# Kernel optimization log

Hardware: AMD Instinct MI355X
Metric: run time of the kernel (lower is better)

## Reference

```python
import jax, jax.numpy as jnp
import numpy as np

# config constants
B, S, H = 4, 2048, 1024
E = 8                 # n_routed_experts
M = 512               # moe_intermediate_size
K = 2                 # num_experts_per_tok
N_SHARED = 2
SM = M * N_SHARED     # shared expert intermediate
G = 64                # gene_size
GE_TEMP = 1.0
ALPHA = 0.001         # aux_loss_alpha
SEQ_AUX = True
NORM_TOPK = True
COS_TEMP = 0.78
CONS_ALPHA = 0.01
LEAKY_SLOPE = 0.01
EPS_COS = 1e-8


def setup_inputs() -> dict:
    key = jax.random.key(0)
    ks = jax.random.split(key, 12)
    sh = 1.0 / np.sqrt(H)
    sm = 1.0 / np.sqrt(M)
    ssm = 1.0 / np.sqrt(SM)
    sg = 1.0 / np.sqrt(G)
    return {
        "hidden_states": jax.random.normal(ks[0], (B, S, H), jnp.float32),
        "g": jax.random.normal(ks[1], (B, G), jnp.float32),
        "wt": jax.random.uniform(ks[2], (E, H), jnp.float32, -sh, sh),   # gate weight_token
        "wg": jax.random.uniform(ks[3], (E, G), jnp.float32, -sg, sg),   # gate weight_gene
        "w_gate": jax.random.uniform(ks[4], (E, H, M), jnp.float32, -sh, sh),
        "w_up": jax.random.uniform(ks[5], (E, H, M), jnp.float32, -sh, sh),
        "w_down": jax.random.uniform(ks[6], (E, M, H), jnp.float32, -sm, sm),
        "sw_gate": jax.random.uniform(ks[7], (H, SM), jnp.float32, -sh, sh),
        "sw_up": jax.random.uniform(ks[8], (H, SM), jnp.float32, -sh, sh),
        "sw_down": jax.random.uniform(ks[9], (SM, H), jnp.float32, -ssm, ssm),
    }


def _leaky(x):
    return jnp.where(x >= 0, x, LEAKY_SLOPE * x)


def _moe_forward(hidden_states, g, wt, wg, w_gate, w_up, w_down, sw_gate, sw_up, sw_down):
    b, s, h = hidden_states.shape
    x = hidden_states.reshape(-1, h)                    # [T, H], T = b*s
    T = x.shape[0]

    # ---- gate ----
    logits_h = x @ wt.T                                 # [T, E]
    logits_g = g @ wg.T                                 # [b, E]
    logits_g = jnp.repeat(logits_g, s, axis=0)          # [T, E]
    logits = (logits_h + logits_g / GE_TEMP) / (1.0 + 1.0 / GE_TEMP)
    scores = jax.nn.softmax(logits, axis=-1)            # [T, E]
    topk_w, topk_idx = jax.lax.top_k(scores, K)         # [T, K]
    if K > 1 and NORM_TOPK:
        topk_w = topk_w / (topk_w.sum(-1, keepdims=True) + 1e-20)

    # aux loss (seq_aux=True)
    onehot = jax.nn.one_hot(topk_idx.reshape(b, s * K), E, dtype=jnp.float32)  # [b, s*K, E]
    ce = onehot.sum(1) / (s * K / E)                    # [b, E]
    aux_loss = (ce * scores.reshape(b, s, E).mean(1)).sum(1).mean() * ALPHA

    # ---- routed experts: dense stacked compute, then gather ----
    gp = _leaky(jnp.einsum('th,ehm->etm', x, w_gate))   # [E, T, M]
    up = jnp.einsum('th,ehm->etm', x, w_up)
    y_all = jnp.einsum('etm,emh->eth', gp * up, w_down) # [E, T, H]
    y_sel = y_all[topk_idx, jnp.arange(T)[:, None], :]  # [T, K, H]
    y = (y_sel * topk_w[..., None]).sum(1).reshape(b, s, h)

    # ---- shared expert ----
    p = (_leaky(hidden_states @ sw_gate) * (hidden_states @ sw_up)) @ sw_down
    y = y + p

    # consistency cosine loss
    num = jnp.sum(y * p, -1)
    den = jnp.maximum(jnp.linalg.norm(y, axis=-1), EPS_COS) * jnp.maximum(jnp.linalg.norm(p, axis=-1), EPS_COS)
    closs = CONS_ALPHA * jnp.mean((num / den) / (1.0 + COS_TEMP))
    return y, aux_loss + closs


def reference(hidden_states, g, wt, wg, w_gate, w_up, w_down, sw_gate, sw_up, sw_down):
    y, _ = _moe_forward(hidden_states, g, wt, wg, w_gate, w_up, w_down, sw_gate, sw_up, sw_down)
    return y
```

## Files before the change

### kernel.cpp

```cpp
#include <hip/hip_runtime.h>
#include <stdint.h>

#define T_TOK 8192
#define H_DIM 1024
#define M_DIM 512
#define SM_DIM 1024
#define E_NUM 8
#define S_SEQ 2048
#define G_DIM 64
#define NASSIGN 16384
#define NSLOT (NASSIGN + E_NUM * 256)
#define MAX_TILES (NASSIGN / 256 + E_NUM)
#define NBLK_PLACE (NASSIGN / 256)

typedef float f32x4 __attribute__((ext_vector_type(4)));
typedef short bf16x8 __attribute__((ext_vector_type(8)));

struct TileDesc { int base; int expert; int nrows; };

#define WAITCNT_VM6 asm volatile("s_waitcnt vmcnt(6)" ::: "memory")
#define WAITCNT_VM4 asm volatile("s_waitcnt vmcnt(4)" ::: "memory")
#define WAITCNT_VM2 asm volatile("s_waitcnt vmcnt(2)" ::: "memory")
#define WAITCNT_VM0 asm volatile("s_waitcnt vmcnt(0)" ::: "memory")

static __device__ __forceinline__ ushort f2b(float f) {
  union { float f; uint32_t u; } a; a.f = f;
  uint32_t r = a.u + 0x7fffu + ((a.u >> 16) & 1u);
  return (ushort)(r >> 16);
}
static __device__ __forceinline__ float b2f(ushort u) {
  union { uint32_t u; float f; } a; a.u = ((uint32_t)u) << 16;
  return a.f;
}
static __device__ __forceinline__ int imin(int a, int b) { return a < b ? a : b; }

static __device__ __forceinline__ void gll16(const void* g, void* l) {
  __builtin_amdgcn_global_load_lds(
      (const __attribute__((address_space(1))) void*)g,
      (__attribute__((address_space(3))) void*)l, 16, 0, 0);
}
static __device__ __forceinline__ int xcd_remap(int wg, int nwg) {
  return (wg & 7) * (nwg >> 3) + (wg >> 3);
}

__global__ __launch_bounds__(256) void prep_kernel(
    const float* __restrict__ x, const float* __restrict__ wt, const float* __restrict__ g,
    const float* __restrict__ wgm,
    const float* __restrict__ w_gate, const float* __restrict__ w_up,
    const float* __restrict__ w_down, const float* __restrict__ sw_gate,
    const float* __restrict__ sw_up, const float* __restrict__ sw_down,
    ushort* __restrict__ wg_t, ushort* __restrict__ wu_t,
    ushort* __restrict__ wd_t, ushort* __restrict__ swg_t,
    ushort* __restrict__ swu_t, ushort* __restrict__ swd_t,
    ushort* __restrict__ xb, int* __restrict__ tidx, float* __restrict__ tw,
    int* __restrict__ bcount) {
  __shared__ float tile[32][33];
  int id = blockIdx.x;
  if (id < 15360) {
    int tx = threadIdx.x & 31, ty = threadIdx.x >> 5;
    const float* src; ushort* dst; int R, C, t;
    if (id < 4096)        { src = w_gate;  dst = wg_t;  R = 1024; C = 512;  t = id; }
    else if (id < 8192)   { src = w_up;    dst = wu_t;  R = 1024; C = 512;  t = id - 4096; }
    else if (id < 12288)  { src = w_down;  dst = wd_t;  R = 512;  C = 1024; t = id - 8192; }
    else if (id < 13312)  { src = sw_gate; dst = swg_t; R = 1024; C = 1024; t = id - 12288; }
    else if (id < 14336)  { src = sw_up;   dst = swu_t; R = 1024; C = 1024; t = id - 13312; }
    else                  { src = sw_down; dst = swd_t; R = 1024; C = 1024; t = id - 14336; }
    int tc = C >> 5;
    int tpm = (R >> 5) * tc;
    int e = t / tpm, tt = t % tpm;
    int c0 = (tt % tc) * 32, r0 = (tt / tc) * 32;
    size_t bo = (size_t)e * R * C;
    src += bo; dst += bo;
#pragma unroll
    for (int i = 0; i < 4; ++i)
      tile[ty + i * 8][tx] = src[(size_t)(r0 + ty + i * 8) * C + c0 + tx];
    __syncthreads();
#pragma unroll
    for (int i = 0; i < 4; ++i)
      dst[(size_t)(c0 + ty + i * 8) * R + r0 + tx] = f2b(tile[tx][ty + i * 8]);
    return;
  }
  int id2 = id - 15360;
  int wv = threadIdx.x >> 6, lane = threadIdx.x & 63;
  int t = id2 * 4 + wv;
  const float4* xr4 = (const float4*)x + (size_t)t * 256;
  ushort4* xb4 = (ushort4*)xb + (size_t)t * 256;
  float a[E_NUM];
#pragma unroll
  for (int e = 0; e < E_NUM; ++e) a[e] = 0.f;
#pragma unroll
  for (int j = 0; j < 4; ++j) {
    float4 v = xr4[lane + 64 * j];
    ushort4 o;
    o.x = f2b(v.x); o.y = f2b(v.y); o.z = f2b(v.z); o.w = f2b(v.w);
    xb4[lane + 64 * j] = o;
#pragma unroll
    for (int e = 0; e < E_NUM; ++e) {
      float4 wv4 = ((const float4*)(wt + (size_t)e * H_DIM))[lane + 64 * j];
      a[e] += v.x * wv4.x + v.y * wv4.y + v.z * wv4.z + v.w * wv4.w;
    }
  }
#pragma unroll
  for (int e = 0; e < E_NUM; ++e)
    for (int off = 32; off; off >>= 1) a[e] += __shfl_xor(a[e], off, 64);
  float lge = 0.f;
  int b = t / S_SEQ;
  if (lane < E_NUM) {
    const float* gv = g + b * G_DIM;
    const float* wv2 = wgm + lane * G_DIM;
    for (int i = 0; i < G_DIM; ++i) lge += gv[i] * wv2[i];
  }
  float l[E_NUM];
#pragma unroll
  for (int e = 0; e < E_NUM; ++e) l[e] = 0.5f * (a[e] + __shfl(lge, e, 64));
  if (lane == 0) {
    int i1 = 0; float b1 = l[0];
#pragma unroll
    for (int e = 1; e < E_NUM; ++e) if (l[e] > b1) { b1 = l[e]; i1 = e; }
    int i2 = -1; float b2 = -1e30f;
#pragma unroll
    for (int e = 0; e < E_NUM; ++e) if (e != i1 && l[e] > b2) { b2 = l[e]; i2 = e; }
    float e2 = expf(b2 - b1);
    float inv = 1.f / (1.f + e2);
    tidx[t * 2] = i1; tidx[t * 2 + 1] = i2;
    tw[t * 2] = inv;  tw[t * 2 + 1] = e2 * inv;
    int chunk = t >> 7;
    atomicAdd(&bcount[chunk * E_NUM + i1], 1);
    atomicAdd(&bcount[chunk * E_NUM + i2], 1);
  }
}

__global__ __launch_bounds__(256) void place2_kernel(
    const int* __restrict__ tidx, const int* __restrict__ bcount,
    int* __restrict__ perm, int* __restrict__ slot_of,
    TileDesc* __restrict__ desc, int* __restrict__ ndesc) {
  __shared__ int cnt[E_NUM];
  __shared__ int myoff[E_NUM];
  __shared__ int wcnt[4][E_NUM];
  int tid = threadIdx.x, wv = tid >> 6, lane = tid & 63, blk = blockIdx.x;
  if (tid < E_NUM) {
    int run = 0, mine = 0;
    for (int b = 0; b < NBLK_PLACE; ++b) {
      if (b == blk) mine = run;
      run += bcount[b * E_NUM + tid];
    }
    cnt[tid] = run;
    myoff[tid] = mine;
  }
  __syncthreads();
  if (tid < E_NUM) {
    int o = 0;
    for (int e = 0; e < tid; ++e) o += cnt[e];
    myoff[tid] += o;
  }
  if (blk == 0 && tid == 32) {
    int o = 0, nd = 0;
    for (int e = 0; e < E_NUM; ++e) {
      int n = cnt[e];
      for (int tb = 0; tb < n; tb += 256) {
        desc[nd].base = o + tb; desc[nd].expert = e;
        desc[nd].nrows = imin(n - tb, 256);
        ++nd;
      }
      o += n;
    }
    *ndesc = nd;
  }
  int i = blk * 256 + tid;
  int e = tidx[i];
  unsigned long long lower = (lane == 63) ? 0x7fffffffffffffffull : ((1ull << lane) - 1ull);
  int rank = 0;
#pragma unroll
  for (int ee = 0; ee < E_NUM; ++ee) {
    unsigned long long m = __ballot(e == ee);
    if (e == ee) rank = __popcll(m & lower);
    if (lane == 0) wcnt[wv][ee] = __popcll(m);
  }
  __syncthreads();
  int off = myoff[e];
  for (int w = 0; w < wv; ++w) off += wcnt[w][e];
  int pos = off + rank;
  perm[pos] = i >> 1;
  slot_of[i] = pos;
}

template <int DUAL>
static __device__ __forceinline__ void gemm_core8(
    const ushort* __restrict__ A, const ushort* __restrict__ B0,
    const ushort* __restrict__ B1, void* __restrict__ Out, int outf32,
    int Kd, int NdOut, int rowbase, int nrows, int n0,
    const int* __restrict__ perm, ushort* __restrict__ LDS) {
  int tid = threadIdx.x, wv = tid >> 6, lane = tid & 63;
  int wr = wv >> 2, wc = wv & 3;
  int lr = lane & 15, cg = lane >> 4;
  int sid = lane >> 3, dch = lane & 7;

  const ushort* apA[2][2];
  const ushort* apB[2][2];
#pragma unroll
  for (int qm = 0; qm < 2; ++qm)
#pragma unroll
    for (int k = 0; k < 2; ++k) {
      int idx = k * 64 + wv * 8 + sid;
      int gch = dch ^ (idx & 7);
      int grow = (idx >> 6) * 128 + qm * 64 + (idx & 63);
      grow = imin(grow, nrows - 1);
      int arow = perm ? perm[rowbase + grow] : rowbase + grow;
      apA[qm][k] = A + (size_t)arow * Kd + gch * 8;
    }
#pragma unroll
  for (int qn = 0; qn < 2; ++qn)
#pragma unroll
    for (int k = 0; k < 2; ++k) {
      int idx = k * 64 + wv * 8 + sid;
      int gch = dch ^ (idx & 7);
      int vrow = n0 + (idx >> 5) * 64 + qn * 32 + (idx & 31);
      const ushort* src; int brow;
      if (DUAL) {
        src = ((vrow >> 4) & 1) ? B1 : B0;
        brow = (vrow >> 5) * 16 + (vrow & 15);
      } else {
        src = B0; brow = vrow;
      }
      apB[qn][k] = src + (size_t)brow * Kd + gch * 8;
    }

  auto stgA = [&](int qm, int k, int nd) {
    gll16(apA[qm][k], LDS + nd * 16384 + qm * 8192 + (k * 512 + wv * 64) * 8);
    apA[qm][k] += 64;
  };
  auto stgB = [&](int qn, int k, int nd) {
    gll16(apB[qn][k], LDS + 32768 + nd * 16384 + qn * 8192 + (k * 512 + wv * 64) * 8);
    apB[qn][k] += 64;
  };
  auto rdA = [&](int d, int qm, int m, int kk) -> bf16x8 {
    int idx = wr * 64 + m * 16 + lr;
    int ch = (kk * 4 + cg) ^ (idx & 7);
    return *(const bf16x8*)(LDS + d * 16384 + qm * 8192 + idx * 64 + ch * 8);
  };
  auto rdB = [&](int d, int qn, int n, int kk) -> bf16x8 {
    int idx = wc * 32 + n * 16 + lr;
    int ch = (kk * 4 + cg) ^ (idx & 7);
    return *(const bf16x8*)(LDS + 32768 + d * 16384 + qn * 8192 + idx * 64 + ch * 8);
  };

  f32x4 acc[2][2][4][2];
#pragma unroll
  for (int qm = 0; qm < 2; ++qm)
#pragma unroll
    for (int qn = 0; qn < 2; ++qn)
#pragma unroll
      for (int m = 0; m < 4; ++m)
#pragma unroll
        for (int n = 0; n < 2; ++n) acc[qm][qn][m][n] = (f32x4){0.f, 0.f, 0.f, 0.f};

  int nk = Kd >> 6;
  stgA(0, 0, 0); stgA(0, 1, 0);
  stgB(0, 0, 0); stgB(0, 1, 0);
  stgB(1, 0, 0); stgB(1, 1, 0);
  stgA(1, 0, 0); stgA(1, 1, 0);
  WAITCNT_VM4;
  __builtin_amdgcn_s_barrier();

  for (int t = 0; t < nk; ++t) {
    int cur = t & 1, nxt = cur ^ 1;
    bool hn = (t + 1 < nk);
    bf16x8 a0f[4][2], a1f[4][2], b0f[2][2], b1f[2][2];

#pragma unroll
    for (int n = 0; n < 2; ++n) { b0f[n][0] = rdB(cur, 0, n, 0); b0f[n][1] = rdB(cur, 0, n, 1); }
#pragma unroll
    for (int m = 0; m < 4; ++m) { a0f[m][0] = rdA(cur, 0, m, 0); a0f[m][1] = rdA(cur, 0, m, 1); }
    if (hn) { stgA(0, 0, nxt); stgA(0, 1, nxt); WAITCNT_VM4; } else { WAITCNT_VM2; }
    __builtin_amdgcn_s_barrier();
    __builtin_amdgcn_s_setprio(1);
#pragma unroll
    for (int m = 0; m < 4; ++m)
#pragma unroll
      for (int n = 0; n < 2; ++n) {
        acc[0][0][m][n] = __builtin_amdgcn_mfma_f32_16x16x32_bf16(a0f[m][0], b0f[n][0], acc[0][0][m][n], 0, 0, 0);
        acc[0][0][m][n] = __builtin_amdgcn_mfma_f32_16x16x32_bf16(a0f[m][1], b0f[n][1], acc[0][0][m][n], 0, 0, 0);
      }
    __builtin_amdgcn_s_setprio(0);

#pragma unroll
    for (int n = 0; n < 2; ++n) { b1f[n][0] = rdB(cur, 1, n, 0); b1f[n][1] = rdB(cur, 1, n, 1); }
    if (hn) { stgB(0, 0, nxt); stgB(0, 1, nxt); WAITCNT_VM4; } else { WAITCNT_VM0; }
    __builtin_amdgcn_s_barrier();
    __builtin_amdgcn_s_setprio(1);
#pragma unroll
    for (int m = 0; m < 4; ++m)
#pragma unroll
      for (int n = 0; n < 2; ++n) {
        acc[0][1][m][n] = __builtin_amdgcn_mfma_f32_16x16x32_bf16(a0f[m][0], b1f[n][0], acc[0][1][m][n], 0, 0, 0);
        acc[0][1][m][n] = __builtin_amdgcn_mfma_f32_16x16x32_bf16(a0f[m][1], b1f[n][1], acc[0][1][m][n], 0, 0, 0);
      }
    __builtin_amdgcn_s_setprio(0);

#pragma unroll
    for (int m = 0; m < 4; ++m) { a1f[m][0] = rdA(cur, 1, m, 0); a1f[m][1] = rdA(cur, 1, m, 1); }
    if (hn) { stgB(1, 0, nxt); stgB(1, 1, nxt); WAITCNT_VM6; }
    __builtin_amdgcn_s_barrier();
    __builtin_amdgcn_s_setprio(1);
#pragma unroll
    for (int m = 0; m < 4; ++m)
#pragma unroll
      for (int n = 0; n < 2; ++n) {
        acc[1][0][m][n] = __builtin_amdgcn_mfma_f32_16x16x32_bf16(a1f[m][0], b0f[n][0], acc[1][0][m][n], 0, 0, 0);
        acc[1][0][m][n] = __builtin_amdgcn_mfma_f32_16x16x32_bf16(a1f[m][1], b0f[n][1], acc[1][0][m][n], 0, 0, 0);
      }
    __builtin_amdgcn_s_setprio(0);

    if (hn) { stgA(1, 0, nxt); stgA(1, 1, nxt); WAITCNT_VM4; }
    __builtin_amdgcn_s_barrier();
    __builtin_amdgcn_s_setprio(1);
#pragma unroll
    for (int m = 0; m < 4; ++m)
#pragma unroll
      for (int n = 0; n < 2; ++n) {
        acc[1][1][m][n] = __builtin_amdgcn_mfma_f32_16x16x32_bf16(a1f[m][0], b1f[n][0], acc[1][1][m][n], 0, 0, 0);
        acc[1][1][m][n] = __builtin_amdgcn_mfma_f32_16x16x32_bf16(a1f[m][1], b1f[n][1], acc[1][1][m][n], 0, 0, 0);
      }
    __builtin_amdgcn_s_setprio(0);
  }

#pragma unroll
  for (int qm = 0; qm < 2; ++qm)
#pragma unroll
    for (int qn = 0; qn < 2; ++qn)
#pragma unroll
      for (int m = 0; m < 4; ++m)
#pragma unroll
        for (int r = 0; r < 4; ++r) {
          int row = wr * 128 + qm * 64 + m * 16 + cg * 4 + r;
          if (row < nrows) {
            if (DUAL) {
              float gv = acc[qm][qn][m][0][r], uv = acc[qm][qn][m][1][r];
              float hv = (gv >= 0.f ? gv : 0.01f * gv) * uv;
              int col = ((n0 >> 5) + wc * 2 + qn) * 16 + lr;
              ((ushort*)Out)[(size_t)(rowbase + row) * NdOut + col] = f2b(hv);
            } else {
#pragma unroll
              for (int n = 0; n < 2; ++n) {
                int col = n0 + wc * 64 + qn * 32 + n * 16 + lr;
                size_t o = (size_t)(rowbase + row) * NdOut + col;
                if (outf32) ((float*)Out)[o] = acc[qm][qn][m][n][r];
                else ((ushort*)Out)[o] = f2b(acc[qm][qn][m][n][r]);
              }
            }
          }
        }
}

__global__ __launch_bounds__(512) void gemm_dual_all(
    const ushort* __restrict__ xb, const ushort* __restrict__ swg,
    const ushort* __restrict__ swu, ushort* __restrict__ hsh,
    const ushort* __restrict__ wg, const ushort* __restrict__ wu,
    ushort* __restrict__ h_e, const int* __restrict__ perm,
    const TileDesc* __restrict__ desc, const int* __restrict__ ndesc) {
  __shared__ ushort LDS[65536];
  int id = xcd_remap(blockIdx.x, gridDim.x);
  if (id < 256) {
    int mt = id >> 3, n0 = (id & 7) * 256;
    gemm_core8<1>(xb, swg, swu, hsh, 0, H_DIM, SM_DIM, mt * 256, 256, n0, nullptr, LDS);
  } else {
    int rid = id - 256;
    int mt = rid >> 2, n0 = (rid & 3) * 256;
    if (mt >= *ndesc) return;
    TileDesc d = desc[mt];
    size_t wo = (size_t)d.expert * M_DIM * H_DIM;
    gemm_core8<1>(xb, wg + wo, wu + wo, h_e, 0, H_DIM, M_DIM, d.base, d.nrows, n0, perm, LDS);
  }
}

__global__ __launch_bounds__(512) void gemm_down_all(
    const ushort* __restrict__ hsh, const ushort* __restrict__ swd, ushort* __restrict__ ysh,
    const ushort* __restrict__ h_e, const ushort* __restrict__ wd, ushort* __restrict__ ye,
    const TileDesc* __restrict__ desc, const int* __restrict__ ndesc) {
  __shared__ ushort LDS[65536];
  int id = xcd_remap(blockIdx.x, gridDim.x);
  if (id < 128) {
    int mt = id >> 2, n0 = (id & 3) * 256;
    gemm_core8<0>(hsh, swd, nullptr, (void*)ysh, 0, SM_DIM, H_DIM, mt * 256, 256, n0, nullptr, LDS);
  } else {
    int rid = id - 128;
    int mt = rid >> 2, n0 = (rid & 3) * 256;
    if (mt >= *ndesc) return;
    TileDesc d = desc[mt];
    gemm_core8<0>(h_e, wd + (size_t)d.expert * H_DIM * M_DIM, nullptr, (void*)ye, 0,
                  M_DIM, H_DIM, d.base, d.nrows, n0, nullptr, LDS);
  }
}

__global__ __launch_bounds__(256) void final_kernel(
    float* __restrict__ y, const ushort* __restrict__ ysh, const ushort* __restrict__ ye,
    const int* __restrict__ slot_of, const float* __restrict__ tw) {
  for (int i = blockIdx.x * 256 + threadIdx.x; i < T_TOK * H_DIM / 4; i += 2048 * 256) {
    int t = i >> 8;
    int c4 = (i & 255) * 4;
    int s0 = slot_of[t * 2], s1 = slot_of[t * 2 + 1];
    float w0 = tw[t * 2], w1 = tw[t * 2 + 1];
    ushort4 pp = *(const ushort4*)(ysh + (size_t)t * H_DIM + c4);
    ushort4 a = *(const ushort4*)(ye + (size_t)s0 * H_DIM + c4);
    ushort4 b = *(const ushort4*)(ye + (size_t)s1 * H_DIM + c4);
    float4 v;
    v.x = b2f(pp.x) + w0 * b2f(a.x) + w1 * b2f(b.x);
    v.y = b2f(pp.y) + w0 * b2f(a.y) + w1 * b2f(b.y);
    v.z = b2f(pp.z) + w0 * b2f(a.z) + w1 * b2f(b.z);
    v.w = b2f(pp.w) + w0 * b2f(a.w) + w1 * b2f(b.w);
    ((float4*)y)[i] = v;
  }
}

extern "C" void kernel_launch(void* const* d_in, const int* in_sizes, int n_in,
                              void* d_out, int out_size, void* d_ws, size_t ws_size,
                              hipStream_t stream) {
  const float* x       = (const float*)d_in[0];
  const float* g       = (const float*)d_in[1];
  const float* wt      = (const float*)d_in[2];
  const float* wg      = (const float*)d_in[3];
  const float* w_gate  = (const float*)d_in[4];
  const float* w_up    = (const float*)d_in[5];
  const float* w_down  = (const float*)d_in[6];
  const float* sw_gate = (const float*)d_in[7];
  const float* sw_up   = (const float*)d_in[8];
  const float* sw_down = (const float*)d_in[9];
  float* y = (float*)d_out;

  char* p = (char*)d_ws;
  auto alloc = [&](size_t bytes) -> char* {
    char* r = p;
    p += (bytes + 255) & ~(size_t)255;
    return r;
  };
  ushort* xb    = (ushort*)alloc((size_t)T_TOK * H_DIM * 2);
  ushort* wg_t  = (ushort*)alloc((size_t)E_NUM * M_DIM * H_DIM * 2);
  ushort* wu_t  = (ushort*)alloc((size_t)E_NUM * M_DIM * H_DIM * 2);
  ushort* wd_t  = (ushort*)alloc((size_t)E_NUM * H_DIM * M_DIM * 2);
  ushort* swg_t = (ushort*)alloc((size_t)SM_DIM * H_DIM * 2);
  ushort* swu_t = (ushort*)alloc((size_t)SM_DIM * H_DIM * 2);
  ushort* swd_t = (ushort*)alloc((size_t)H_DIM * SM_DIM * 2);
  int* tidx     = (int*)alloc(NASSIGN * 4);
  float* tw     = (float*)alloc(NASSIGN * 4);
  int* bcount   = (int*)alloc(NBLK_PLACE * E_NUM * 4);
  int* ndesc    = (int*)alloc(4);
  int* perm     = (int*)alloc(NASSIGN * 4);
  int* slot_of  = (int*)alloc(NASSIGN * 4);
  TileDesc* desc = (TileDesc*)alloc(MAX_TILES * sizeof(TileDesc));
  ushort* h_e   = (ushort*)alloc((size_t)NSLOT * M_DIM * 2);
  ushort* hsh   = (ushort*)alloc((size_t)T_TOK * SM_DIM * 2);
  ushort* ye    = (ushort*)alloc((size_t)NSLOT * H_DIM * 2);
  ushort* ysh   = (ushort*)alloc((size_t)T_TOK * H_DIM * 2);
  (void)ws_size; (void)in_sizes; (void)n_in; (void)out_size;

  hipMemsetAsync(bcount, 0, NBLK_PLACE * E_NUM * 4, stream);
  prep_kernel<<<15360 + 2048, 256, 0, stream>>>(
      x, wt, g, wg, w_gate, w_up, w_down, sw_gate, sw_up, sw_down,
      wg_t, wu_t, wd_t, swg_t, swu_t, swd_t, xb, tidx, tw, bcount);
  place2_kernel<<<NBLK_PLACE, 256, 0, stream>>>(tidx, bcount, perm, slot_of, desc, ndesc);

  gemm_dual_all<<<256 + MAX_TILES * 4, 512, 0, stream>>>(
      xb, swg_t, swu_t, hsh, wg_t, wu_t, h_e, perm, desc, ndesc);
  gemm_down_all<<<128 + MAX_TILES * 4, 512, 0, stream>>>(
      hsh, swd_t, ysh, h_e, wd_t, ye, desc, ndesc);

  final_kernel<<<2048, 256, 0, stream>>>(y, ysh, ye, slot_of, tw);
}
```

Baseline: 212.8 us.

## Widen weight transpose tiles and make dual GEMM a persistent work loop

The weight transpose/convert in prep_kernel now uses 64x64 tiles with float4 loads and ushort4 stores, so it launches a quarter as many blocks and issues wider memory accesses. The gate/up dual GEMM becomes a persistent kernel with a fixed grid of 512 blocks that loops over the shared-expert and routed-expert tiles up to the actual tile count. This replaces the oversized grid whose surplus blocks exited immediately. The risk is that the 512-block grid may balance work across CUs less evenly. The larger padded LDS tile and the fixed remap window also change the access patterns.

```diff
diff --git a/kernel.cpp b/kernel.cpp
--- a/kernel.cpp
+++ b/kernel.cpp
@@ -12,6 +12,7 @@
 #define NSLOT (NASSIGN + E_NUM * 256)
 #define MAX_TILES (NASSIGN / 256 + E_NUM)
 #define NBLK_PLACE (NASSIGN / 256)
+#define NT_W 3840
 
 typedef float f32x4 __attribute__((ext_vector_type(4)));
 typedef short bf16x8 __attribute__((ext_vector_type(8)));
@@ -54,34 +55,44 @@
     ushort* __restrict__ swu_t, ushort* __restrict__ swd_t,
     ushort* __restrict__ xb, int* __restrict__ tidx, float* __restrict__ tw,
     int* __restrict__ bcount) {
-  __shared__ float tile[32][33];
+  __shared__ float tile[64][65];
   int id = blockIdx.x;
-  if (id < 15360) {
-    int tx = threadIdx.x & 31, ty = threadIdx.x >> 5;
+  int tid = threadIdx.x;
+  if (id < NT_W) {
+    int tx = tid & 15, ty = tid >> 4;
     const float* src; ushort* dst; int R, C, t;
-    if (id < 4096)        { src = w_gate;  dst = wg_t;  R = 1024; C = 512;  t = id; }
-    else if (id < 8192)   { src = w_up;    dst = wu_t;  R = 1024; C = 512;  t = id - 4096; }
-    else if (id < 12288)  { src = w_down;  dst = wd_t;  R = 512;  C = 1024; t = id - 8192; }
-    else if (id < 13312)  { src = sw_gate; dst = swg_t; R = 1024; C = 1024; t = id - 12288; }
-    else if (id < 14336)  { src = sw_up;   dst = swu_t; R = 1024; C = 1024; t = id - 13312; }
-    else                  { src = sw_down; dst = swd_t; R = 1024; C = 1024; t = id - 14336; }
-    int tc = C >> 5;
-    int tpm = (R >> 5) * tc;
+    if (id < 1024)        { src = w_gate;  dst = wg_t;  R = 1024; C = 512;  t = id; }
+    else if (id < 2048)   { src = w_up;    dst = wu_t;  R = 1024; C = 512;  t = id - 1024; }
+    else if (id < 3072)   { src = w_down;  dst = wd_t;  R = 512;  C = 1024; t = id - 2048; }
+    else if (id < 3328)   { src = sw_gate; dst = swg_t; R = 1024; C = 1024; t = id - 3072; }
+    else if (id < 3584)   { src = sw_up;   dst = swu_t; R = 1024; C = 1024; t = id - 3328; }
+    else                  { src = sw_down; dst = swd_t; R = 1024; C = 1024; t = id - 3584; }
+    int tc = C >> 6;
+    int tpm = (R >> 6) * tc;
     int e = t / tpm, tt = t % tpm;
-    int c0 = (tt % tc) * 32, r0 = (tt / tc) * 32;
+    int c0 = (tt % tc) * 64, r0 = (tt / tc) * 64;
     size_t bo = (size_t)e * R * C;
     src += bo; dst += bo;
 #pragma unroll
-    for (int i = 0; i < 4; ++i)
-      tile[ty + i * 8][tx] = src[(size_t)(r0 + ty + i * 8) * C + c0 + tx];
+    for (int p = 0; p < 4; ++p) {
+      int row = ty + p * 16;
+      float4 v = *(const float4*)&src[(size_t)(r0 + row) * C + c0 + tx * 4];
+      tile[row][tx * 4 + 0] = v.x; tile[row][tx * 4 + 1] = v.y;
+      tile[row][tx * 4 + 2] = v.z; tile[row][tx * 4 + 3] = v.w;
+    }
     __syncthreads();
 #pragma unroll
-    for (int i = 0; i < 4; ++i)
-      dst[(size_t)(c0 + ty + i * 8) * R + r0 + tx] = f2b(tile[tx][ty + i * 8]);
+    for (int p = 0; p < 4; ++p) {
+      int cc = ty + p * 16;
+      ushort4 o;
+      o.x = f2b(tile[tx * 4 + 0][cc]); o.y = f2b(tile[tx * 4 + 1][cc]);
+      o.z = f2b(tile[tx * 4 + 2][cc]); o.w = f2b(tile[tx * 4 + 3][cc]);
+      *(ushort4*)&dst[(size_t)(c0 + cc) * R + r0 + tx * 4] = o;
+    }
     return;
   }
-  int id2 = id - 15360;
-  int wv = threadIdx.x >> 6, lane = threadIdx.x & 63;
+  int id2 = id - NT_W;
+  int wv = tid >> 6, lane = tid & 63;
   int t = id2 * 4 + wv;
   const float4* xr4 = (const float4*)x + (size_t)t * 256;
   ushort4* xb4 = (ushort4*)xb + (size_t)t * 256;
@@ -359,17 +370,20 @@
     ushort* __restrict__ h_e, const int* __restrict__ perm,
     const TileDesc* __restrict__ desc, const int* __restrict__ ndesc) {
   __shared__ ushort LDS[65536];
-  int id = xcd_remap(blockIdx.x, gridDim.x);
-  if (id < 256) {
-    int mt = id >> 3, n0 = (id & 7) * 256;
-    gemm_core8<1>(xb, swg, swu, hsh, 0, H_DIM, SM_DIM, mt * 256, 256, n0, nullptr, LDS);
-  } else {
-    int rid = id - 256;
-    int mt = rid >> 2, n0 = (rid & 3) * 256;
-    if (mt >= *ndesc) return;
-    TileDesc d = desc[mt];
-    size_t wo = (size_t)d.expert * M_DIM * H_DIM;
-    gemm_core8<1>(xb, wg + wo, wu + wo, h_e, 0, H_DIM, M_DIM, d.base, d.nrows, n0, perm, LDS);
+  int nit = 256 + 4 * (*ndesc);
+  for (int v = blockIdx.x; v < nit; v += gridDim.x) {
+    int id = (v < 512) ? xcd_remap(v, 512) : v;
+    if (id < 256) {
+      int mt = id >> 3, n0 = (id & 7) * 256;
+      gemm_core8<1>(xb, swg, swu, hsh, 0, H_DIM, SM_DIM, mt * 256, 256, n0, nullptr, LDS);
+    } else {
+      int rid = id - 256;
+      int mt = rid >> 2, n0 = (rid & 3) * 256;
+      TileDesc d = desc[mt];
+      size_t wo = (size_t)d.expert * M_DIM * H_DIM;
+      gemm_core8<1>(xb, wg + wo, wu + wo, h_e, 0, H_DIM, M_DIM, d.base, d.nrows, n0, perm, LDS);
+    }
+    __builtin_amdgcn_s_barrier();
   }
 }
 
@@ -454,12 +468,12 @@
   (void)ws_size; (void)in_sizes; (void)n_in; (void)out_size;
 
   hipMemsetAsync(bcount, 0, NBLK_PLACE * E_NUM * 4, stream);
-  prep_kernel<<<15360 + 2048, 256, 0, stream>>>(
+  prep_kernel<<<NT_W + 2048, 256, 0, stream>>>(
       x, wt, g, wg, w_gate, w_up, w_down, sw_gate, sw_up, sw_down,
       wg_t, wu_t, wd_t, swg_t, swu_t, swd_t, xb, tidx, tw, bcount);
   place2_kernel<<<NBLK_PLACE, 256, 0, stream>>>(tidx, bcount, perm, slot_of, desc, ndesc);
 
-  gemm_dual_all<<<256 + MAX_TILES * 4, 512, 0, stream>>>(
+  gemm_dual_all<<<512, 512, 0, stream>>>(
       xb, swg_t, swu_t, hsh, wg_t, wu_t, h_e, perm, desc, ndesc);
   gemm_down_all<<<128 + MAX_TILES * 4, 512, 0, stream>>>(
       hsh, swd_t, ysh, h_e, wd_t, ye, desc, ndesc);
```

After: 217.5 us. 1.02x slower.
